# Performance work log

Measured on AMD Instinct MI355X. Metric: run time of the kernel, lower is better.

## Reference

```python
import jax, jax.numpy as jnp
import numpy as np

GAMMA = 0.5
ITERATIONS = 1


def setup_inputs() -> dict:
    key = jax.random.key(0)
    # x: [batch, heads, num_windows, N, dim]
    x = jax.random.normal(key, (4, 8, 64, 256, 128), dtype=jnp.float32)
    return {"x": x}


def _l2norm(v):
    return v / jnp.linalg.norm(v, axis=-1, keepdims=True)


def _get_codebook(x):
    # x: [b,h,w,n,d] -> c: [b,h,w,d]
    B, H, W, N, D = x.shape
    c = _l2norm(jnp.sum(x, axis=-2))              # init: window mean direction
    xf = x.reshape(B, H, W * N, D)                # flatten windows: [b,h,l,d], l = W*N
    for _ in range(ITERATIONS):
        aff = jnp.einsum('bhnd,bhld->bhnl', c, xf)           # [b,h,W,W*N]
        a_hw = jax.nn.one_hot(jnp.argmax(aff, axis=-1), W * N, dtype=x.dtype)  # [b,h,W,W*N]
        a_n = jax.nn.one_hot(jnp.argmax(aff, axis=-2), W, dtype=x.dtype)       # [b,h,W*N,W]
        attn = a_hw + jnp.swapaxes(a_n, -2, -1)              # [b,h,W,W*N]
        delta_c = _l2norm(jnp.einsum('bhnl,bhld->bhnd', attn, xf))
        c = _l2norm(GAMMA * c + (1.0 - GAMMA) * delta_c)
    return c


def reference(x):
    # x: [b,h,w,n,d]
    W = x.shape[2]
    c = _get_codebook(x)                                     # [b,h,w,d]
    cos_sim = jnp.einsum('bhrcd,bhsd->bhrcs', x, c)          # [b,h,w,n,w]
    delta_onehot = jax.nn.one_hot(jnp.argmax(cos_sim, axis=-1), W, dtype=jnp.float32)
    return delta_onehot, c
```

## Files before the change

### kernel.cpp

```cpp
#include <hip/hip_runtime.h>

typedef unsigned long long u64;
typedef unsigned int u32;

#define G_ 32
#define L_ 16384
#define D_ 128
#define ONEHOT_ 33554432LL

__global__ __launch_bounds__(256) void k1_sums(const float* __restrict__ x,
                                               float* __restrict__ c0n) {
  int blk = blockIdx.x;
  const float* xp = x + ((size_t)blk << 15);
  int t = threadIdx.x;
  int d4 = t & 31, r0 = t >> 5;
  float4 acc = make_float4(0.f, 0.f, 0.f, 0.f);
  #pragma unroll 4
  for (int r = r0; r < 256; r += 8) {
    float4 v = *(const float4*)(xp + r * D_ + d4 * 4);
    acc.x += v.x; acc.y += v.y; acc.z += v.z; acc.w += v.w;
  }
  __shared__ float4 part[8][32];
  __shared__ double ssq[33];
  part[r0][d4] = acc;
  __syncthreads();
  if (t < 32) {
    float4 s = part[0][t];
    for (int r = 1; r < 8; ++r) {
      float4 v = part[r][t];
      s.x += v.x; s.y += v.y; s.z += v.z; s.w += v.w;
    }
    part[0][t] = s;
    ssq[t] = (double)s.x * s.x + (double)s.y * s.y + (double)s.z * s.z + (double)s.w * s.w;
  }
  __syncthreads();
  if (t == 0) {
    double tot = 0.0;
    for (int i = 0; i < 32; ++i) tot += ssq[i];
    ssq[32] = 1.0 / sqrt(tot);
  }
  __syncthreads();
  if (t < 32) {
    float rn = (float)ssq[32];
    float4 s = part[0][t];
    float4 c = make_float4(s.x * rn, s.y * rn, s.z * rn, s.w * rn);
    *(float4*)(c0n + ((size_t)blk << 7) + t * 4) = c;
  }
}

__global__ __launch_bounds__(512)
void k2_assign(const float* __restrict__ x,
               const float* __restrict__ c0n,
               u64* __restrict__ deltaI,
               u64* __restrict__ best) {
  __shared__ float4 cL[64 * 33];
  __shared__ float4 xq[8][16 * 9];
  __shared__ u64 ldsD[64 * 130];
  int g = blockIdx.x >> 3, bsub = blockIdx.x & 7;
  int t = threadIdx.x, lane = t & 63, wv = t >> 6;
  int l15 = lane & 15, pg = lane >> 4;
  const float* xg = x + ((size_t)g << 21);
  const float4* cg4 = (const float4*)(c0n + ((size_t)g << 13));
  for (int i = t; i < 2048; i += 512)
    cL[(i >> 5) * 33 + (i & 31)] = cg4[i];
  for (int i = t; i < 64 * 130; i += 512) ldsD[i] = 0ULL;
  __syncthreads();

  float4* xw = xq[wv];
  int sp = lane >> 2, sh = lane & 3;

  float rbv[4]; int rbp[4];
  #pragma unroll
  for (int s = 0; s < 4; ++s) { rbv[s] = -3.0e38f; rbp[s] = 0; }

  int wbase = bsub * 2048 + wv * 256;
  for (int tile = 0; tile < 16; ++tile) {
    int p0 = wbase + tile * 16;
    float4 acc[4][4];
    #pragma unroll
    for (int s = 0; s < 4; ++s)
      #pragma unroll
      for (int j = 0; j < 4; ++j) acc[s][j] = make_float4(0.f, 0.f, 0.f, 0.f);

    for (int q = 0; q < 4; ++q) {
      const float4* gsrc = (const float4*)(xg + ((size_t)(p0 + sp) << 7) + (q << 5));
      float4* xrow = xw + sp * 9;
      xrow[sh * 2]     = gsrc[sh * 2];
      xrow[sh * 2 + 1] = gsrc[sh * 2 + 1];
      #pragma unroll
      for (int d4l = 0; d4l < 8; ++d4l) {
        float4 ca[4];
        #pragma unroll
        for (int s = 0; s < 4; ++s)
          ca[s] = cL[(l15 + (s << 4)) * 33 + (q << 3) + d4l];
        #pragma unroll
        for (int j = 0; j < 4; ++j) {
          float4 xv = xw[(pg * 4 + j) * 9 + d4l];
          #pragma unroll
          for (int s = 0; s < 4; ++s) {
            acc[s][j].x += ca[s].x * xv.x;
            acc[s][j].y += ca[s].y * xv.y;
            acc[s][j].z += ca[s].z * xv.z;
            acc[s][j].w += ca[s].w * xv.w;
          }
        }
      }
    }

    int w1s[4];
    #pragma unroll
    for (int j = 0; j < 4; ++j) {
      int p = p0 + pg * 4 + j;
      float av[4];
      #pragma unroll
      for (int s = 0; s < 4; ++s)
        av[s] = (acc[s][j].x + acc[s][j].y) + (acc[s][j].z + acc[s][j].w);
      #pragma unroll
      for (int s = 0; s < 4; ++s)
        if (av[s] > rbv[s]) { rbv[s] = av[s]; rbp[s] = p; }
      float v1 = av[0]; int w1 = l15;
      #pragma unroll
      for (int s = 1; s < 4; ++s)
        if (av[s] > v1) { v1 = av[s]; w1 = l15 + (s << 4); }
      #pragma unroll
      for (int off = 1; off <= 8; off <<= 1) {
        float ov = __shfl_xor(v1, off); int ow = __shfl_xor(w1, off);
        if (ov > v1 || (ov == v1 && ow < w1)) { v1 = ov; w1 = ow; }
      }
      w1s[j] = w1;
    }

    #pragma unroll
    for (int i = 0; i < 16; ++i) {
      int w1p = __shfl(w1s[i & 3], (i >> 2) << 4);
      const float* xr = xg + ((size_t)(p0 + i) << 7);
      float va = xr[lane];
      float vb = xr[lane + 64];
      u64* dst = ldsD + w1p * 130 + lane;
      atomicAdd(dst, (u64)(long long)__double2ll_rn((double)va * 4294967296.0));
      atomicAdd(dst + 64, (u64)(long long)__double2ll_rn((double)vb * 4294967296.0));
    }
  }

  #pragma unroll
  for (int s = 0; s < 4; ++s) {
    #pragma unroll
    for (int off = 16; off <= 32; off <<= 1) {
      float ov = __shfl_xor(rbv[s], off); int op = __shfl_xor(rbp[s], off);
      if (ov > rbv[s] || (ov == rbv[s] && op < rbp[s])) { rbv[s] = ov; rbp[s] = op; }
    }
  }
  if (pg == 0) {
    #pragma unroll
    for (int s = 0; s < 4; ++s) {
      u32 key = __float_as_uint(rbv[s]);
      key ^= (key & 0x80000000u) ? 0xFFFFFFFFu : 0x80000000u;
      u64 pk = ((u64)key << 32) | (u64)(0xFFFFFFFFu - (u32)rbp[s]);
      atomicMax(&best[(g << 6) + l15 + (s << 4)], pk);
    }
  }

  __syncthreads();
  for (int i = t; i < 8192; i += 512) {
    u64 v = ldsD[(i >> 7) * 130 + (i & 127)];
    if (v) atomicAdd(&deltaI[((size_t)g << 13) + i], v);
  }
}

__global__ __launch_bounds__(128) void k3_final(const float* __restrict__ x,
                                                const float* __restrict__ c0n,
                                                const u64* __restrict__ deltaI,
                                                const u64* __restrict__ best,
                                                float* __restrict__ cOut,
                                                float* __restrict__ c2n) {
  int blk = blockIdx.x, g = blk >> 6;
  int d = threadIdx.x;
  u64 pk = best[blk];
  int bl = (int)(0xFFFFFFFFu - (u32)(pk & 0xFFFFFFFFull));
  float xb = x[((size_t)g << 21) + ((size_t)bl << 7) + d];
  long long di = (long long)deltaI[((size_t)blk << 7) + d];
  double delta = (double)di * (1.0 / 4294967296.0) + (double)xb;

  __shared__ double red[128];
  __shared__ double inv;
  red[d] = delta * delta;
  __syncthreads();
  for (int s = 64; s > 0; s >>= 1) {
    if (d < s) red[d] += red[d + s];
    __syncthreads();
  }
  if (d == 0) inv = 1.0 / sqrt(red[0]);
  __syncthreads();
  float dn = (float)(delta * inv);
  float b2 = 0.5f * c0n[((size_t)blk << 7) + d] + 0.5f * dn;
  __syncthreads();
  red[d] = (double)b2 * b2;
  __syncthreads();
  for (int s = 64; s > 0; s >>= 1) {
    if (d < s) red[d] += red[d + s];
    __syncthreads();
  }
  if (d == 0) inv = 1.0 / sqrt(red[0]);
  __syncthreads();
  float cf = b2 * (float)inv;
  cOut[((size_t)blk << 7) + d] = cf;
  c2n[((size_t)blk << 7) + d] = cf;
}

__global__ __launch_bounds__(512)
void k4_onehot(const float* __restrict__ x,
               const float* __restrict__ c2n,
               float* __restrict__ out) {
  __shared__ float4 cL[64 * 33];
  __shared__ float4 xq[8][16 * 9];
  int g = blockIdx.x >> 4, bsub = blockIdx.x & 15;
  int t = threadIdx.x, lane = t & 63, wv = t >> 6;
  int l15 = lane & 15, pg = lane >> 4;
  const float* xg = x + ((size_t)g << 21);
  const float4* cg4 = (const float4*)(c2n + ((size_t)g << 13));
  for (int i = t; i < 2048; i += 512)
    cL[(i >> 5) * 33 + (i & 31)] = cg4[i];
  __syncthreads();

  float4* xw = xq[wv];
  int sp = lane >> 2, sh = lane & 3;

  int wbase = bsub * 1024 + wv * 128;
  for (int tile = 0; tile < 8; ++tile) {
    int p0 = wbase + tile * 16;
    float4 acc[4][4];
    #pragma unroll
    for (int s = 0; s < 4; ++s)
      #pragma unroll
      for (int j = 0; j < 4; ++j) acc[s][j] = make_float4(0.f, 0.f, 0.f, 0.f);

    for (int q = 0; q < 4; ++q) {
      const float4* gsrc = (const float4*)(xg + ((size_t)(p0 + sp) << 7) + (q << 5));
      float4* xrow = xw + sp * 9;
      xrow[sh * 2]     = gsrc[sh * 2];
      xrow[sh * 2 + 1] = gsrc[sh * 2 + 1];
      #pragma unroll
      for (int d4l = 0; d4l < 8; ++d4l) {
        float4 ca[4];
        #pragma unroll
        for (int s = 0; s < 4; ++s)
          ca[s] = cL[(l15 + (s << 4)) * 33 + (q << 3) + d4l];
        #pragma unroll
        for (int j = 0; j < 4; ++j) {
          float4 xv = xw[(pg * 4 + j) * 9 + d4l];
          #pragma unroll
          for (int s = 0; s < 4; ++s) {
            acc[s][j].x += ca[s].x * xv.x;
            acc[s][j].y += ca[s].y * xv.y;
            acc[s][j].z += ca[s].z * xv.z;
            acc[s][j].w += ca[s].w * xv.w;
          }
        }
      }
    }

    #pragma unroll
    for (int j = 0; j < 4; ++j) {
      int p = p0 + pg * 4 + j;
      float av[4];
      #pragma unroll
      for (int s = 0; s < 4; ++s)
        av[s] = (acc[s][j].x + acc[s][j].y) + (acc[s][j].z + acc[s][j].w);
      float v1 = av[0]; int w1 = l15;
      #pragma unroll
      for (int s = 1; s < 4; ++s)
        if (av[s] > v1) { v1 = av[s]; w1 = l15 + (s << 4); }
      #pragma unroll
      for (int off = 1; off <= 8; off <<= 1) {
        float ov = __shfl_xor(v1, off); int ow = __shfl_xor(w1, off);
        if (ov > v1 || (ov == v1 && ow < w1)) { v1 = ov; w1 = ow; }
      }
      int w0 = l15 << 2;
      float4 vv;
      vv.x = (w1 == w0    ) ? 1.f : 0.f;
      vv.y = (w1 == w0 + 1) ? 1.f : 0.f;
      vv.z = (w1 == w0 + 2) ? 1.f : 0.f;
      vv.w = (w1 == w0 + 3) ? 1.f : 0.f;
      *(float4*)(out + (((size_t)(g * L_ + p)) << 6) + w0) = vv;
    }
  }
}

extern "C" void kernel_launch(void* const* d_in, const int* in_sizes, int n_in,
                              void* d_out, int out_size, void* d_ws, size_t ws_size,
                              hipStream_t stream) {
  const float* x = (const float*)d_in[0];
  float* out = (float*)d_out;
  float* cOut = out + ONEHOT_;
  char* ws = (char*)d_ws;
  float* c0n   = (float*)(ws);
  float* c2n   = (float*)(ws + (1u << 20));
  u64*  deltaI = (u64*)(ws + (3u << 20));
  u64*  best   = (u64*)(ws + (5u << 20));

  hipMemsetAsync(ws + (3u << 20), 0, (2u << 20) + 16384, stream);

  hipLaunchKernelGGL(k1_sums,   dim3(2048), dim3(256), 0, stream, x, c0n);
  hipLaunchKernelGGL(k2_assign, dim3(256),  dim3(512), 0, stream, x, c0n, deltaI, best);
  hipLaunchKernelGGL(k3_final,  dim3(2048), dim3(128), 0, stream,
                     x, c0n, deltaI, best, cOut, c2n);
  hipLaunchKernelGGL(k4_onehot, dim3(512),  dim3(512), 0, stream, x, c2n, out);
}
```

Baseline: 477.6 us.

## Split assignment and delta accumulation into separate kernels, double block count

The assign kernel no longer does LDS atomic accumulation of x rows into per-codeword sums. It writes packed byte argmax indices to a workspace buffer, and a new kernel reads them back to do the fixed-point atomic accumulation. Both kernels now launch 512 blocks, each covering half as many points, to raise occupancy and free the large LDS buffer from the assign kernel. The cost is an extra kernel launch, a second read of x from global memory, and twice as many global atomic flushes of the per-block delta.

```diff
diff --git a/kernel.cpp b/kernel.cpp
--- a/kernel.cpp
+++ b/kernel.cpp
@@ -51,19 +51,17 @@
 __global__ __launch_bounds__(512)
 void k2_assign(const float* __restrict__ x,
                const float* __restrict__ c0n,
-               u64* __restrict__ deltaI,
+               u32* __restrict__ aPack,
                u64* __restrict__ best) {
   __shared__ float4 cL[64 * 33];
   __shared__ float4 xq[8][16 * 9];
-  __shared__ u64 ldsD[64 * 130];
-  int g = blockIdx.x >> 3, bsub = blockIdx.x & 7;
+  int g = blockIdx.x >> 4, bsub = blockIdx.x & 15;
   int t = threadIdx.x, lane = t & 63, wv = t >> 6;
   int l15 = lane & 15, pg = lane >> 4;
   const float* xg = x + ((size_t)g << 21);
   const float4* cg4 = (const float4*)(c0n + ((size_t)g << 13));
   for (int i = t; i < 2048; i += 512)
     cL[(i >> 5) * 33 + (i & 31)] = cg4[i];
-  for (int i = t; i < 64 * 130; i += 512) ldsD[i] = 0ULL;
   __syncthreads();
 
   float4* xw = xq[wv];
@@ -73,8 +71,8 @@
   #pragma unroll
   for (int s = 0; s < 4; ++s) { rbv[s] = -3.0e38f; rbp[s] = 0; }
 
-  int wbase = bsub * 2048 + wv * 256;
-  for (int tile = 0; tile < 16; ++tile) {
+  int wbase = bsub * 1024 + wv * 128;
+  for (int tile = 0; tile < 8; ++tile) {
     int p0 = wbase + tile * 16;
     float4 acc[4][4];
     #pragma unroll
@@ -130,15 +128,10 @@
       w1s[j] = w1;
     }
 
-    #pragma unroll
-    for (int i = 0; i < 16; ++i) {
-      int w1p = __shfl(w1s[i & 3], (i >> 2) << 4);
-      const float* xr = xg + ((size_t)(p0 + i) << 7);
-      float va = xr[lane];
-      float vb = xr[lane + 64];
-      u64* dst = ldsD + w1p * 130 + lane;
-      atomicAdd(dst, (u64)(long long)__double2ll_rn((double)va * 4294967296.0));
-      atomicAdd(dst + 64, (u64)(long long)__double2ll_rn((double)vb * 4294967296.0));
+    if (l15 == 0) {
+      u32 pk4 = (u32)w1s[0] | ((u32)w1s[1] << 8) |
+                ((u32)w1s[2] << 16) | ((u32)w1s[3] << 24);
+      aPack[((g * L_ + p0) >> 2) + pg] = pk4;
     }
   }
 
@@ -158,6 +151,32 @@
       u64 pk = ((u64)key << 32) | (u64)(0xFFFFFFFFu - (u32)rbp[s]);
       atomicMax(&best[(g << 6) + l15 + (s << 4)], pk);
     }
+  }
+}
+
+__global__ __launch_bounds__(512)
+void k2d_delta(const float* __restrict__ x,
+               const u32* __restrict__ aPack,
+               u64* __restrict__ deltaI) {
+  __shared__ u64 ldsD[64 * 130];
+  int g = blockIdx.x >> 4, bsub = blockIdx.x & 15;
+  int t = threadIdx.x, lane = t & 63, wv = t >> 6;
+  const float* xg = x + ((size_t)g << 21);
+  for (int i = t; i < 64 * 130; i += 512) ldsD[i] = 0ULL;
+  __syncthreads();
+
+  int pbase = bsub * 1024 + wv * 128;
+  #pragma unroll 4
+  for (int i = 0; i < 128; ++i) {
+    int p = pbase + i;
+    u32 pk4 = aPack[(g * L_ + p) >> 2];
+    int aw = (int)((pk4 >> ((p & 3) * 8)) & 63u);
+    const float* xr = xg + ((size_t)p << 7);
+    float va = xr[lane];
+    float vb = xr[lane + 64];
+    u64* dst = ldsD + aw * 130 + lane;
+    atomicAdd(dst, (u64)(long long)__double2ll_rn((double)va * 4294967296.0));
+    atomicAdd(dst + 64, (u64)(long long)__double2ll_rn((double)vb * 4294967296.0));
   }
 
   __syncthreads();
@@ -297,11 +316,13 @@
   float* c2n   = (float*)(ws + (1u << 20));
   u64*  deltaI = (u64*)(ws + (3u << 20));
   u64*  best   = (u64*)(ws + (5u << 20));
+  u32*  aPack  = (u32*)(ws + (5u << 20) + 65536);
 
   hipMemsetAsync(ws + (3u << 20), 0, (2u << 20) + 16384, stream);
 
   hipLaunchKernelGGL(k1_sums,   dim3(2048), dim3(256), 0, stream, x, c0n);
-  hipLaunchKernelGGL(k2_assign, dim3(256),  dim3(512), 0, stream, x, c0n, deltaI, best);
+  hipLaunchKernelGGL(k2_assign, dim3(512),  dim3(512), 0, stream, x, c0n, aPack, best);
+  hipLaunchKernelGGL(k2d_delta, dim3(512),  dim3(512), 0, stream, x, aPack, deltaI);
   hipLaunchKernelGGL(k3_final,  dim3(2048), dim3(128), 0, stream,
                      x, c0n, deltaI, best, cOut, c2n);
   hipLaunchKernelGGL(k4_onehot, dim3(512),  dim3(512), 0, stream, x, c2n, out);
```

Result: slower. 489.9 us (+2.6%).
